# Performance work log

Measured on AMD Instinct MI355X. Metric: run time of the kernel, lower is better.

The kernel has to match this reference:

```python
import jax, jax.numpy as jnp
import numpy as np

N = 50000      # nodes
E = 800000     # edges
T = 3          # npass
ED = 64        # embedding_dim
NS = 23        # nshifts (arange(0.8, 3.0+1e-5, 0.1))
MD = NS + ED   # message_dim = 87
H = 200        # hidden width (hardcoded in module)
NMOL = 2048    # number of molecules (segments for final scatter)
RD = ED * (T + 1)  # readout input dim = 256
EPS = 1e-5

SHIFTS = jnp.asarray(np.arange(0.8, 3.0 + 1e-5, 0.1, dtype=np.float32))  # [23]


def setup_inputs() -> dict:
    key = jax.random.key(0)
    ks = jax.random.split(key, 32)
    inp = {
        'z_i': jax.random.randint(ks[0], (N,), 0, 10),
        'edge_index': jax.random.randint(ks[1], (2, E), 0, N),
        'dist_ij': jax.random.uniform(ks[2], (E, 1), dtype=jnp.float32) * 2.2 + 0.8,
        'mol_ind': jnp.sort(jax.random.randint(ks[3], (N,), 0, NMOL)),
        'emb': jax.random.normal(ks[4], (10, ED), dtype=jnp.float32),
        # per-pass update MLP params, stacked over T
        'up_bn_g': jnp.ones((T, MD), jnp.float32),
        'up_bn_b': jnp.zeros((T, MD), jnp.float32),
        'up_w1': jax.random.normal(ks[5], (T, MD, H), jnp.float32) * 0.05,
        'up_b1': jnp.zeros((T, H), jnp.float32),
        'up_w2': jax.random.normal(ks[6], (T, H, H), jnp.float32) * 0.05,
        'up_b2': jnp.zeros((T, H), jnp.float32),
        'up_w3': jax.random.normal(ks[7], (T, H, H), jnp.float32) * 0.05,
        'up_b3': jnp.zeros((T, H), jnp.float32),
        'up_w4': jax.random.normal(ks[8], (T, H, ED), jnp.float32) * 0.05,
        'up_b4': jnp.zeros((T, ED), jnp.float32),
        # readout MLP params
        'ro_bn_g': jnp.ones((RD,), jnp.float32),
        'ro_bn_b': jnp.zeros((RD,), jnp.float32),
        'ro_w1': jax.random.normal(ks[9], (RD, H), jnp.float32) * 0.05,
        'ro_b1': jnp.zeros((H,), jnp.float32),
        'ro_w2': jax.random.normal(ks[10], (H, H), jnp.float32) * 0.05,
        'ro_b2': jnp.zeros((H,), jnp.float32),
        'ro_w3': jax.random.normal(ks[11], (H, H), jnp.float32) * 0.05,
        'ro_b3': jnp.zeros((H,), jnp.float32),
        'ro_w4': jax.random.normal(ks[12], (H, 1), jnp.float32) * 0.05,
        'ro_b4': jnp.zeros((1,), jnp.float32),  # bias filled to 0 in __init__
    }
    return inp


def batchnorm(x, g, b):
    # BatchNorm1d in training mode: batch statistics, biased variance
    mu = jnp.mean(x, axis=0)
    var = jnp.mean(jnp.square(x - mu), axis=0)
    return (x - mu) * jax.lax.rsqrt(var + EPS) * g + b


def mlp(x, g, b, w1, b1, w2, b2, w3, b3, w4, b4):
    x = batchnorm(x, g, b)
    x = jax.nn.relu(x @ w1 + b1)
    x = jax.nn.relu(x @ w2 + b2)
    x = jax.nn.relu(x @ w3 + b3)
    return x @ w4 + b4


def reference(z_i, edge_index, dist_ij, mol_ind, emb,
              up_bn_g, up_bn_b, up_w1, up_b1, up_w2, up_b2, up_w3, up_b3, up_w4, up_b4,
              ro_bn_g, ro_bn_b, ro_w1, ro_b1, ro_w2, ro_b2, ro_w3, ro_b3, ro_w4, ro_b4):
    e_source, e_sink = edge_index[0], edge_index[1]
    rbf_ij = jnp.exp(-jnp.square(dist_ij - SHIFTS[None, :]))  # [E, NS]
    x_i = emb[z_i]                                            # [N, ED]
    x_list = [x_i]
    for t in range(T):
        m_ij = jnp.concatenate([rbf_ij, x_i[e_sink]], axis=1)  # [E, MD] gather
        m_i = jax.ops.segment_sum(m_ij, e_source, num_segments=N)  # scatter-sum
        x_i = x_i + 0.1 * mlp(m_i, up_bn_g[t], up_bn_b[t],
                              up_w1[t], up_b1[t], up_w2[t], up_b2[t],
                              up_w3[t], up_b3[t], up_w4[t], up_b4[t])
        x_list.append(x_i)
    x_all = jnp.concatenate(x_list, axis=1)  # [N, RD]
    y_i = mlp(x_all, ro_bn_g, ro_bn_b, ro_w1, ro_b1, ro_w2, ro_b2, ro_w3, ro_b3, ro_w4, ro_b4)
    y = jax.ops.segment_sum(y_i, mol_ind, num_segments=NMOL)  # [NMOL, 1]
    return y
```

## Files before the change

kernel.cpp:

```cpp
#include <hip/hip_runtime.h>
#include <hip/hip_bf16.h>
#include <type_traits>

#define NN 50000
#define NP 50048
#define EE 800000
#define TT 3
#define ED 64
#define NS 23
#define MD 87
#define HH 200
#define NMOL 2048
#define RD 256

#define SW 264
#define NPB2 512
#define SNB ((NN + 255) / 256)

typedef __attribute__((ext_vector_type(8))) short short8b;
typedef __attribute__((ext_vector_type(4))) float f32x4;

template <int V> using ic = std::integral_constant<int, V>;

__device__ __forceinline__ unsigned short f2bf(float f) {
  unsigned u = __float_as_uint(f);
  return (unsigned short)((u + 0x7fffu + ((u >> 16) & 1u)) >> 16);
}
__device__ __forceinline__ float ubf2f(unsigned short h) {
  return __uint_as_float(((unsigned)h) << 16);
}
__device__ __forceinline__ float bfp2f(unsigned p) {
  return __uint_as_float(p << 16) + __uint_as_float(p & 0xffff0000u);
}
__device__ __forceinline__ unsigned packsplit(float v) {
  unsigned short h = f2bf(v);
  unsigned short l = f2bf(v - ubf2f(h));
  return (unsigned)h | ((unsigned)l << 16);
}

__device__ __forceinline__ void gl2lds16(const short* g, short* l) {
  __builtin_amdgcn_global_load_lds(
      (const __attribute__((address_space(1))) unsigned int*)g,
      (__attribute__((address_space(3))) unsigned int*)l, 16, 0, 0);
}

__device__ __forceinline__ void vmwait(int n) {
  switch (n) {
    case 0: asm volatile("s_waitcnt vmcnt(0)" ::: "memory"); break;
    case 1: asm volatile("s_waitcnt vmcnt(1)" ::: "memory"); break;
    case 2: asm volatile("s_waitcnt vmcnt(2)" ::: "memory"); break;
    case 3: asm volatile("s_waitcnt vmcnt(3)" ::: "memory"); break;
    default: asm volatile("s_waitcnt vmcnt(4)" ::: "memory"); break;
  }
}

struct WD { const float* src; short* dst; int K, N, Kpad, Npad, T; };
struct WDs { WD d[5]; };

__global__ __launch_bounds__(256) void wprep_kernel(WDs W) {
  WD w = W.d[blockIdx.y];
  int KB = w.Kpad >> 5, NT = w.Npad >> 4;
  int per = w.Npad * w.Kpad;
  int total = w.T * per;
  for (int idx = blockIdx.x * 256 + threadIdx.x; idx < total; idx += gridDim.x * 256) {
    int t = idx / per;
    int r = idx - t * per;
    int e = r & 7, lane = (r >> 3) & 63;
    int blk = r >> 9;
    int kb = blk % KB, tile = blk / KB;
    int ln = lane & 15, quad = lane >> 4;
    int n = tile * 16 + ln, k = kb * 32 + quad * 8 + e;
    float v = 0.f;
    if (k < w.K && n < w.N) v = w.src[((size_t)t * w.K + k) * w.N + n];
    unsigned short h = f2bf(v);
    unsigned short l = f2bf(v - ubf2f(h));
    size_t base = ((size_t)(t * NT + tile) * KB + kb) * 1024;
    w.dst[base + lane * 8 + e] = (short)h;
    w.dst[base + 512 + lane * 8 + e] = (short)l;
  }
}

__global__ __launch_bounds__(256) void wscale_kernel(const float* __restrict__ wsrc,
                                                     const float* __restrict__ na,
                                                     const float* __restrict__ nb,
                                                     const float* __restrict__ bsrc,
                                                     int K, int Kpad,
                                                     short* __restrict__ wsp,
                                                     float* __restrict__ bc) {
  int n = blockIdx.x;
  int k = threadIdx.x;
  int KB = Kpad >> 5;
  int tile = n >> 4, ln = n & 15;
  float contrib = 0.f;
  if (k < Kpad) {
    float v = 0.f;
    if (n < HH && k < K) {
      float w = wsrc[(size_t)k * HH + n];
      v = na[k] * w;
      contrib = nb[k] * w;
    }
    unsigned short h = f2bf(v);
    unsigned short l = f2bf(v - ubf2f(h));
    int kb = k >> 5, quad = (k & 31) >> 3, e = k & 7;
    int lane = quad * 16 + ln;
    size_t base = ((size_t)tile * KB + kb) * 1024;
    wsp[base + lane * 8 + e] = (short)h;
    wsp[base + 512 + lane * 8 + e] = (short)l;
  }
  __shared__ float sh[256];
  sh[k] = contrib;
  __syncthreads();
  for (int off = 128; off > 0; off >>= 1) {
    if (k < off) sh[k] += sh[k + off];
    __syncthreads();
  }
  if (k == 0) bc[n] = (n < HH ? bsrc[n] : 0.f) + sh[0];
}

__global__ __launch_bounds__(256) void emb_kernel(const int* __restrict__ z,
                                                  const float* __restrict__ emb,
                                                  unsigned* __restrict__ xp,
                                                  short* __restrict__ xq,
                                                  short* __restrict__ xqs) {
  int idx = blockIdx.x * 256 + threadIdx.x;
  if (idx >= NN * ED) return;
  int i = idx >> 6, d = idx & 63;
  unsigned pk = packsplit(emb[z[i] * ED + d]);
  xp[(size_t)i * RD + d] = pk;
  short h = (short)(pk & 0xffffu);
  xq[(size_t)i * RD + d] = h;
  xqs[(size_t)i * ED + d] = h;
}

__global__ __launch_bounds__(256) void hist_kernel(const int* __restrict__ src,
                                                   int* __restrict__ deg) {
  int e = blockIdx.x * 256 + threadIdx.x;
  if (e < EE) atomicAdd(&deg[src[e]], 1);
}

__global__ __launch_bounds__(256) void scanA_kernel(const int* __restrict__ deg,
                                                    int* __restrict__ Psum) {
  int i = blockIdx.x * 256 + threadIdx.x;
  int v = (i < NN) ? deg[i] : 0;
#pragma unroll
  for (int off = 32; off > 0; off >>= 1) v += __shfl_down(v, off, 64);
  __shared__ int ws[4];
  if ((threadIdx.x & 63) == 0) ws[threadIdx.x >> 6] = v;
  __syncthreads();
  if (threadIdx.x == 0) Psum[blockIdx.x] = ws[0] + ws[1] + ws[2] + ws[3];
}

__global__ __launch_bounds__(256) void scanB_kernel(const int* __restrict__ Psum,
                                                    int* __restrict__ Poff) {
  __shared__ int sh[256];
  int t = threadIdx.x;
  int v = (t < SNB) ? Psum[t] : 0;
  sh[t] = v;
  __syncthreads();
  for (int off = 1; off < 256; off <<= 1) {
    int u = (t >= off) ? sh[t - off] : 0;
    __syncthreads();
    sh[t] += u;
    __syncthreads();
  }
  if (t < SNB) Poff[t] = sh[t] - v;
}

__global__ __launch_bounds__(256) void scanC_kernel(const int* __restrict__ deg,
                                                    const int* __restrict__ Poff,
                                                    int* __restrict__ offs,
                                                    int* __restrict__ cursor) {
  __shared__ int sh[256];
  int t = threadIdx.x;
  int i = blockIdx.x * 256 + t;
  int v = (i < NN) ? deg[i] : 0;
  sh[t] = v;
  __syncthreads();
  for (int off = 1; off < 256; off <<= 1) {
    int u = (t >= off) ? sh[t - off] : 0;
    __syncthreads();
    sh[t] += u;
    __syncthreads();
  }
  int excl = Poff[blockIdx.x] + sh[t] - v;
  if (i < NN) {
    offs[i] = excl;
    cursor[i] = excl;
    if (i == NN - 1) offs[NN] = excl + v;
  }
}

__global__ __launch_bounds__(256) void scatter_kernel(const int* __restrict__ src,
                                                      const int* __restrict__ snk,
                                                      const float* __restrict__ dist,
                                                      int* __restrict__ cursor,
                                                      int* __restrict__ ssink,
                                                      float* __restrict__ sdist) {
  int e = blockIdx.x * 256 + threadIdx.x;
  if (e >= EE) return;
  int p = atomicAdd(&cursor[src[e]], 1);
  ssink[p] = snk[e];
  sdist[p] = dist[e];
}

template <bool RBF>
__global__ __launch_bounds__(256) void gather_kernel(const int* __restrict__ offs,
                                                     const int* __restrict__ ssink,
                                                     const float* __restrict__ sdist,
                                                     const short* __restrict__ xqs,
                                                     short* __restrict__ mh) {
  int node = blockIdx.x * 4 + (threadIdx.x >> 6);
  int lane = threadIdx.x & 63;
  if (node >= NN) return;
  float shift = (float)(0.8 + 0.1 * (double)lane);
  int e0 = offs[node], e1 = offs[node + 1];
  float ax0 = 0.f, ax1 = 0.f, ar0 = 0.f, ar1 = 0.f;
  int j = e0;
  for (; j + 4 <= e1; j += 4) {
    int s0 = ssink[j], s1 = ssink[j + 1], s2 = ssink[j + 2], s3 = ssink[j + 3];
    float x0 = ubf2f((unsigned short)xqs[(size_t)s0 * ED + lane]);
    float x1 = ubf2f((unsigned short)xqs[(size_t)s1 * ED + lane]);
    float x2 = ubf2f((unsigned short)xqs[(size_t)s2 * ED + lane]);
    float x3 = ubf2f((unsigned short)xqs[(size_t)s3 * ED + lane]);
    ax0 += x0 + x2;
    ax1 += x1 + x3;
    if (RBF && lane < NS) {
      float d0 = sdist[j], d1 = sdist[j + 1], d2 = sdist[j + 2], d3 = sdist[j + 3];
      float u0 = d0 - shift, u1 = d1 - shift, u2 = d2 - shift, u3 = d3 - shift;
      ar0 += __expf(-u0 * u0) + __expf(-u2 * u2);
      ar1 += __expf(-u1 * u1) + __expf(-u3 * u3);
    }
  }
  for (; j < e1; j++) {
    int s = ssink[j];
    ax0 += ubf2f((unsigned short)xqs[(size_t)s * ED + lane]);
    if (RBF && lane < NS) {
      float u = sdist[j] - shift;
      ar0 += __expf(-u * u);
    }
  }
  float accx = ax0 + ax1;
  if (RBF && lane < NS) mh[(size_t)node * 96 + lane] = (short)f2bf(ar0 + ar1);
  if (RBF && lane >= NS && lane < 32) mh[(size_t)node * 96 + 64 + lane] = 0;
  mh[(size_t)node * 96 + NS + lane] = (short)f2bf(accx);
}

template <int LD>
__global__ __launch_bounds__(256) void colstats_s16_kernel(const short* __restrict__ X,
                                                           float* __restrict__ P) {
  constexpr int CG = LD / 8;
  constexpr int RPB = 256 / CG;
  const int t = threadIdx.x;
  const int cg = t % CG, rin = t / CG;
  float s[8] = {0, 0, 0, 0, 0, 0, 0, 0}, q[8] = {0, 0, 0, 0, 0, 0, 0, 0};
  if (rin < RPB) {
    for (int r = blockIdx.x * RPB + rin; r < NN; r += gridDim.x * RPB) {
      union { uint4 v; short e[8]; } u;
      u.v = *(const uint4*)(X + (size_t)r * LD + cg * 8);
#pragma unroll
      for (int e = 0; e < 8; e++) {
        float f = ubf2f((unsigned short)u.e[e]);
        s[e] += f;
        q[e] += f * f;
      }
    }
  }
  __shared__ float sh[256][16];
#pragma unroll
  for (int e = 0; e < 8; e++) { sh[t][e] = s[e]; sh[t][8 + e] = q[e]; }
  __syncthreads();
  if (rin == 0) {
    for (int rr = 1; rr < RPB; rr++) {
      const float* o = sh[rr * CG + cg];
#pragma unroll
      for (int e = 0; e < 8; e++) { s[e] += o[e]; q[e] += o[8 + e]; }
    }
    float* Pb = P + blockIdx.x * 512;
#pragma unroll
    for (int e = 0; e < 8; e++) {
      Pb[cg * 8 + e] = s[e];
      Pb[256 + cg * 8 + e] = q[e];
    }
  }
}

__global__ __launch_bounds__(256) void bnfinal2_kernel(const float* __restrict__ P, int nblk,
                                                       const float* __restrict__ g,
                                                       const float* __restrict__ b, int ncols,
                                                       float* __restrict__ na,
                                                       float* __restrict__ nb) {
  int c = blockIdx.x;
  int t = threadIdx.x;
  float s = 0.f, q = 0.f;
  for (int i = t; i < nblk; i += 256) {
    s += P[i * 512 + c];
    q += P[i * 512 + 256 + c];
  }
#pragma unroll
  for (int off = 32; off > 0; off >>= 1) {
    s += __shfl_down(s, off, 64);
    q += __shfl_down(q, off, 64);
  }
  __shared__ float ws[4], wq[4];
  if ((t & 63) == 0) { ws[t >> 6] = s; wq[t >> 6] = q; }
  __syncthreads();
  if (t == 0) {
    s = ws[0] + ws[1] + ws[2] + ws[3];
    q = wq[0] + wq[1] + wq[2] + wq[3];
    if (c < ncols) {
      float mean = s / (float)NN;
      float var = q / (float)NN - mean * mean;
      float a = g[c] * rsqrtf(var + 1e-5f);
      na[c] = a;
      nb[c] = b[c] - mean * a;
    } else {
      na[c] = 0.f;
      nb[c] = 0.f;
    }
  }
}

template <bool READOUT>
__global__ __launch_bounds__(256, 2) void fused_kernel(
    const short* __restrict__ Agh,
    const short* __restrict__ W1p, const short* __restrict__ W2p,
    const short* __restrict__ W3p, const short* __restrict__ W4p,
    const float* __restrict__ b1, const float* __restrict__ b2,
    const float* __restrict__ b3, const float* __restrict__ b4,
    unsigned* __restrict__ xp, short* __restrict__ xq, short* __restrict__ xqs,
    int t, const float* __restrict__ w4ro, const int* __restrict__ mol,
    float* __restrict__ out) {
  __shared__ short act[64 * SW];
  __shared__ short bufW[3][13 * 512];
  constexpr int GLDA = READOUT ? RD : 96;
  constexpr int KB1 = READOUT ? 8 : 3;
  const int tid = threadIdx.x;
  const int wave = tid >> 6, lane = tid & 63, ln = lane & 15, quad = lane >> 4;
  const int q8 = quad * 8;
  const int bm = blockIdx.x * 64;

  if constexpr (!READOUT) {
#pragma unroll
    for (int i = 0; i < 3; i++) {
      int idx = tid + 256 * i;
      int row = idx / 12, col = (idx - row * 12) * 8;
      *(uint4*)(act + row * SW + col) =
          *(const uint4*)(Agh + (size_t)(bm + row) * GLDA + col);
    }
    {
      int row = tid >> 2, c = 208 + (tid & 3) * 4;
      *(uint2*)(act + row * SW + c) = (uint2){0u, 0u};
    }
  } else {
#pragma unroll
    for (int i = 0; i < 8; i++) {
      int idx = tid + 256 * i;
      int row = idx >> 5, col = (idx & 31) * 8;
      *(uint4*)(act + row * SW + col) =
          *(const uint4*)(Agh + (size_t)(bm + row) * GLDA + col);
    }
  }
  __syncthreads();

  f32x4 acc[4][4];
  short8b a[4];

  auto stage = [&](const short* __restrict__ Wp, int NT, int KB, int TERMS,
                   int s, int bi) {
    int kb = (TERMS == 2) ? (s >> 1) : s;
    int pl = (TERMS == 2) ? ((s & 1) << 9) : 0;
    short* dst = &bufW[bi][0];
#pragma unroll
    for (int j = 0; j < 4; j++) {
      int tile = wave + 4 * j;
      if (tile < NT)
        gl2lds16(Wp + (size_t)(tile * KB + kb) * 1024 + pl + lane * 8,
                 dst + tile * 512);
    }
  };

  auto runloop = [&](auto ntt, auto kbt, auto tt, const short* __restrict__ Wp) {
    constexpr int NT = decltype(ntt)::value;
    constexpr int KB = decltype(kbt)::value;
    constexpr int TERMS = decltype(tt)::value;
    constexpr int NSL = KB * TERMS;
    constexpr int NJ = (NT + 3) >> 2;
    const int ntw = (NT - wave + 3) >> 2;
#pragma unroll
    for (int j = 0; j < NJ; j++)
#pragma unroll
      for (int i = 0; i < 4; i++) acc[j][i] = (f32x4){0.f, 0.f, 0.f, 0.f};
#pragma unroll
    for (int s = 0; s < NSL; s++) {
      vmwait((s < NSL - 1) ? ntw : 0);
      __builtin_amdgcn_s_barrier();
      __builtin_amdgcn_sched_barrier(0);
      if (s + 2 < NSL) stage(Wp, NT, KB, TERMS, s + 2, (s + 2) % 3);
      if (TERMS == 1 || (s & 1) == 0) {
        const int kb = (TERMS == 2) ? (s >> 1) : s;
#pragma unroll
        for (int i = 0; i < 4; i++)
          a[i] = *(const short8b*)(act + (i * 16 + ln) * SW + kb * 32 + q8);
      }
      const short* bw = &bufW[s % 3][0];
#pragma unroll
      for (int j = 0; j < NJ; j++) {
        int tile = wave + 4 * j;
        if (tile < NT) {
          short8b b = *(const short8b*)(bw + tile * 512 + lane * 8);
#pragma unroll
          for (int i = 0; i < 4; i++)
            acc[j][i] =
                __builtin_amdgcn_mfma_f32_16x16x32_bf16(a[i], b, acc[j][i], 0, 0, 0);
        }
      }
    }
  };

  auto epi = [&](auto ntt, const float* __restrict__ bias) {
    constexpr int NT = decltype(ntt)::value;
    constexpr int NJ = (NT + 3) >> 2;
#pragma unroll
    for (int j = 0; j < NJ; j++) {
      int tile = wave + 4 * j;
      if (tile < NT) {
        int colg = tile * 16 + ln;
        float bb = (colg < HH) ? bias[colg] : 0.f;
#pragma unroll
        for (int i = 0; i < 4; i++)
#pragma unroll
          for (int r = 0; r < 4; r++)
            act[(i * 16 + quad * 4 + r) * SW + colg] =
                (short)f2bf(fmaxf(acc[j][i][r] + bb, 0.f));
      }
    }
  };

  auto lgkmbar = [&]() {
    asm volatile("s_waitcnt lgkmcnt(0)" ::: "memory");
    __builtin_amdgcn_s_barrier();
    __builtin_amdgcn_sched_barrier(0);
  };

  stage(W1p, 13, KB1, 2, 0, 0);
  stage(W1p, 13, KB1, 2, 1, 1);
  runloop(ic<13>{}, ic<KB1>{}, ic<2>{}, W1p);
  __builtin_amdgcn_s_barrier();
  __builtin_amdgcn_sched_barrier(0);
  stage(W2p, 13, 7, 1, 0, 0);
  stage(W2p, 13, 7, 1, 1, 1);
  epi(ic<13>{}, b1);
  lgkmbar();

  runloop(ic<13>{}, ic<7>{}, ic<1>{}, W2p);
  __builtin_amdgcn_s_barrier();
  __builtin_amdgcn_sched_barrier(0);
  stage(W3p, 13, 7, 1, 0, 0);
  stage(W3p, 13, 7, 1, 1, 1);
  epi(ic<13>{}, b2);
  lgkmbar();

  runloop(ic<13>{}, ic<7>{}, ic<1>{}, W3p);
  __builtin_amdgcn_s_barrier();
  __builtin_amdgcn_sched_barrier(0);

  if constexpr (!READOUT) {
    stage(W4p, 4, 7, 2, 0, 0);
    stage(W4p, 4, 7, 2, 1, 1);
    epi(ic<13>{}, b3);
    lgkmbar();
    runloop(ic<4>{}, ic<7>{}, ic<2>{}, W4p);
    int colg = wave * 16 + ln;
    float bb = b4[colg];
#pragma unroll
    for (int i = 0; i < 4; i++)
#pragma unroll
      for (int r = 0; r < 4; r++) {
        int grow = bm + i * 16 + quad * 4 + r;
        if (grow < NN) {
          size_t base = (size_t)grow * RD;
          float oldv = bfp2f(xp[base + (size_t)t * ED + colg]);
          unsigned pk = packsplit(oldv + 0.1f * (acc[0][i][r] + bb));
          xp[base + (size_t)(t + 1) * ED + colg] = pk;
          short h = (short)(pk & 0xffffu);
          xq[base + (size_t)(t + 1) * ED + colg] = h;
          xqs[(size_t)(t + 1) * NN * ED + (size_t)grow * ED + colg] = h;
        }
      }
  } else {
    epi(ic<13>{}, b3);
    lgkmbar();
    int row = tid >> 2;
    float s = 0.f;
    for (int c = (tid & 3); c < HH; c += 4)
      s += ubf2f((unsigned short)act[row * SW + c]) * w4ro[c];
    s += __shfl_xor(s, 1, 64);
    s += __shfl_xor(s, 2, 64);
    int grow = bm + row;
    if ((tid & 3) == 0 && grow < NN) atomicAdd(&out[mol[grow]], s + b4[0]);
  }
}

extern "C" void kernel_launch(void* const* d_in, const int* in_sizes, int n_in,
                              void* d_out, int out_size, void* d_ws, size_t ws_size,
                              hipStream_t stream) {
  const int* z_i = (const int*)d_in[0];
  const int* e_src = (const int*)d_in[1];
  const int* e_snk = ((const int*)d_in[1]) + EE;
  const float* dist = (const float*)d_in[2];
  const int* mol = (const int*)d_in[3];
  const float* emb = (const float*)d_in[4];
  const float* up_bn_g = (const float*)d_in[5];
  const float* up_bn_b = (const float*)d_in[6];
  const float* up_w1 = (const float*)d_in[7];
  const float* up_b1 = (const float*)d_in[8];
  const float* up_w2 = (const float*)d_in[9];
  const float* up_b2 = (const float*)d_in[10];
  const float* up_w3 = (const float*)d_in[11];
  const float* up_b3 = (const float*)d_in[12];
  const float* up_w4 = (const float*)d_in[13];
  const float* up_b4 = (const float*)d_in[14];
  const float* ro_bn_g = (const float*)d_in[15];
  const float* ro_bn_b = (const float*)d_in[16];
  const float* ro_w1 = (const float*)d_in[17];
  const float* ro_b1 = (const float*)d_in[18];
  const float* ro_w2 = (const float*)d_in[19];
  const float* ro_b2 = (const float*)d_in[20];
  const float* ro_w3 = (const float*)d_in[21];
  const float* ro_b3 = (const float*)d_in[22];
  const float* ro_w4 = (const float*)d_in[23];
  const float* ro_b4 = (const float*)d_in[24];
  float* out = (float*)d_out;

  char* p = (char*)d_ws;
  auto alloc = [&](size_t bytes) {
    void* r = (void*)p;
    p += (bytes + 255) & ~(size_t)255;
    return r;
  };
  unsigned* x_p = (unsigned*)alloc((size_t)NN * RD * 4);
  short* x_q = (short*)alloc((size_t)NP * RD * 2);
  short* x_qs = (short*)alloc((size_t)(TT + 1) * NN * ED * 2);
  short* mh = (short*)alloc((size_t)NP * 96 * 2);
  int* ssink = (int*)alloc((size_t)EE * 4);
  float* sdist = (float*)alloc((size_t)EE * 4);
  int* offs = (int*)alloc((size_t)(NN + 1) * 4);
  int* deg = (int*)alloc((size_t)NN * 4);
  int* cursor = (int*)alloc((size_t)NN * 4);
  int* Psum = (int*)alloc((size_t)SNB * 4);
  int* Poff = (int*)alloc((size_t)SNB * 4);
  float* P = (float*)alloc((size_t)NPB2 * 512 * 4);
  float* na = (float*)alloc(256 * 4);
  float* nb = (float*)alloc(256 * 4);
  float* b1c = (float*)alloc(208 * 4);
  short* w1sp = (short*)alloc((size_t)13 * 3 * 1024 * 2);
  short* r1sp = (short*)alloc((size_t)13 * 8 * 1024 * 2);
  short* w2p = (short*)alloc((size_t)TT * 13 * 7 * 1024 * 2);
  short* w3p = (short*)alloc((size_t)TT * 13 * 7 * 1024 * 2);
  short* w4p = (short*)alloc((size_t)TT * 4 * 7 * 1024 * 2);
  short* r2p = (short*)alloc((size_t)13 * 7 * 1024 * 2);
  short* r3p = (short*)alloc((size_t)13 * 7 * 1024 * 2);

  hipMemsetAsync(deg, 0, (size_t)NN * 4, stream);
  hipMemsetAsync(out, 0, (size_t)NMOL * 4, stream);

  WDs descs;
  descs.d[0] = {up_w2, w2p, HH, HH, 224, 208, TT};
  descs.d[1] = {up_w3, w3p, HH, HH, 224, 208, TT};
  descs.d[2] = {up_w4, w4p, HH, ED, 224, 64, TT};
  descs.d[3] = {ro_w2, r2p, HH, HH, 224, 208, 1};
  descs.d[4] = {ro_w3, r3p, HH, HH, 224, 208, 1};
  wprep_kernel<<<dim3(546, 5), 256, 0, stream>>>(descs);

  emb_kernel<<<(NN * ED + 255) / 256, 256, 0, stream>>>(z_i, emb, x_p, x_q, x_qs);
  hist_kernel<<<(EE + 255) / 256, 256, 0, stream>>>(e_src, deg);
  scanA_kernel<<<SNB, 256, 0, stream>>>(deg, Psum);
  scanB_kernel<<<1, 256, 0, stream>>>(Psum, Poff);
  scanC_kernel<<<SNB, 256, 0, stream>>>(deg, Poff, offs, cursor);
  scatter_kernel<<<(EE + 255) / 256, 256, 0, stream>>>(e_src, e_snk, dist, cursor, ssink, sdist);

  const int gM = NP / 64;

  for (int t = 0; t < TT; t++) {
    if (t == 0)
      gather_kernel<true><<<(NN + 3) / 4, 256, 0, stream>>>(
          offs, ssink, sdist, x_qs, mh);
    else
      gather_kernel<false><<<(NN + 3) / 4, 256, 0, stream>>>(
          offs, ssink, sdist, x_qs + (size_t)t * NN * ED, mh);
    colstats_s16_kernel<96><<<NPB2, 256, 0, stream>>>(mh, P);
    bnfinal2_kernel<<<256, 256, 0, stream>>>(P, NPB2, up_bn_g + t * MD, up_bn_b + t * MD, MD,
                                             na, nb);
    wscale_kernel<<<208, 256, 0, stream>>>(up_w1 + (size_t)t * MD * HH, na, nb,
                                           up_b1 + t * HH, MD, 96, w1sp, b1c);
    fused_kernel<false><<<gM, 256, 0, stream>>>(
        mh, w1sp,
        w2p + (size_t)t * 13 * 7 * 1024, w3p + (size_t)t * 13 * 7 * 1024,
        w4p + (size_t)t * 4 * 7 * 1024,
        b1c, up_b2 + t * HH, up_b3 + t * HH, up_b4 + t * ED,
        x_p, x_q, x_qs, t, nullptr, nullptr, nullptr);
  }

  colstats_s16_kernel<256><<<NPB2, 256, 0, stream>>>(x_q, P);
  bnfinal2_kernel<<<256, 256, 0, stream>>>(P, NPB2, ro_bn_g, ro_bn_b, RD, na, nb);
  wscale_kernel<<<208, 256, 0, stream>>>(ro_w1, na, nb, ro_b1, RD, 256, r1sp, b1c);
  fused_kernel<true><<<gM, 256, 0, stream>>>(
      x_q, r1sp, r2p, r3p, nullptr,
      b1c, ro_b2, ro_b3, ro_b4,
      nullptr, nullptr, nullptr, 0, ro_w4, mol, out);

  (void)in_sizes; (void)n_in; (void)out_size; (void)ws_size;
}
```

Measured before the change: 612.7 us.

## Simplify fused MLP pipeline to double buffering with higher occupancy

Replaces the triple-buffered, template-specialized weight pipeline with a runtime-parameterized double-buffered loop synchronized by __syncthreads each step. It shrinks the activation stride and weight buffers to cut LDS usage and raises the occupancy hint to three blocks per CU. The first layer now reads A fragments directly from global memory instead of staging them in LDS. It trades explicit vmcnt-based overlap and compile-time unrolling for lower LDS footprint, risking less latency hiding and possible async-load ordering issues.

```diff
diff --git a/kernel.cpp b/kernel.cpp
--- a/kernel.cpp
+++ b/kernel.cpp
@@ -13,14 +13,12 @@
 #define NMOL 2048
 #define RD 256
 
-#define SW 264
+#define SW 216
 #define NPB2 512
 #define SNB ((NN + 255) / 256)
 
 typedef __attribute__((ext_vector_type(8))) short short8b;
 typedef __attribute__((ext_vector_type(4))) float f32x4;
-
-template <int V> using ic = std::integral_constant<int, V>;
 
 __device__ __forceinline__ unsigned short f2bf(float f) {
   unsigned u = __float_as_uint(f);
@@ -42,16 +40,6 @@
   __builtin_amdgcn_global_load_lds(
       (const __attribute__((address_space(1))) unsigned int*)g,
       (__attribute__((address_space(3))) unsigned int*)l, 16, 0, 0);
-}
-
-__device__ __forceinline__ void vmwait(int n) {
-  switch (n) {
-    case 0: asm volatile("s_waitcnt vmcnt(0)" ::: "memory"); break;
-    case 1: asm volatile("s_waitcnt vmcnt(1)" ::: "memory"); break;
-    case 2: asm volatile("s_waitcnt vmcnt(2)" ::: "memory"); break;
-    case 3: asm volatile("s_waitcnt vmcnt(3)" ::: "memory"); break;
-    default: asm volatile("s_waitcnt vmcnt(4)" ::: "memory"); break;
-  }
 }
 
 struct WD { const float* src; short* dst; int K, N, Kpad, Npad, T; };
@@ -321,7 +309,7 @@
 }
 
 template <bool READOUT>
-__global__ __launch_bounds__(256, 2) void fused_kernel(
+__global__ __launch_bounds__(256, 3) void fused_kernel(
     const short* __restrict__ Agh,
     const short* __restrict__ W1p, const short* __restrict__ W2p,
     const short* __restrict__ W3p, const short* __restrict__ W4p,
@@ -331,7 +319,7 @@
     int t, const float* __restrict__ w4ro, const int* __restrict__ mol,
     float* __restrict__ out) {
   __shared__ short act[64 * SW];
-  __shared__ short bufW[3][13 * 512];
+  __shared__ short bufW[2][13 * 512];
   constexpr int GLDA = READOUT ? RD : 96;
   constexpr int KB1 = READOUT ? 8 : 3;
   const int tid = threadIdx.x;
@@ -339,72 +327,48 @@
   const int q8 = quad * 8;
   const int bm = blockIdx.x * 64;
 
-  if constexpr (!READOUT) {
-#pragma unroll
-    for (int i = 0; i < 3; i++) {
-      int idx = tid + 256 * i;
-      int row = idx / 12, col = (idx - row * 12) * 8;
-      *(uint4*)(act + row * SW + col) =
-          *(const uint4*)(Agh + (size_t)(bm + row) * GLDA + col);
-    }
-    {
-      int row = tid >> 2, c = 208 + (tid & 3) * 4;
-      *(uint2*)(act + row * SW + c) = (uint2){0u, 0u};
-    }
-  } else {
-#pragma unroll
-    for (int i = 0; i < 8; i++) {
-      int idx = tid + 256 * i;
-      int row = idx >> 5, col = (idx & 31) * 8;
-      *(uint4*)(act + row * SW + col) =
-          *(const uint4*)(Agh + (size_t)(bm + row) * GLDA + col);
-    }
-  }
-  __syncthreads();
-
   f32x4 acc[4][4];
-  short8b a[4];
+  const short8b zfrag = {0, 0, 0, 0, 0, 0, 0, 0};
 
   auto stage = [&](const short* __restrict__ Wp, int NT, int KB, int TERMS,
-                   int s, int bi) {
+                   int s, int b) {
     int kb = (TERMS == 2) ? (s >> 1) : s;
     int pl = (TERMS == 2) ? ((s & 1) << 9) : 0;
-    short* dst = &bufW[bi][0];
 #pragma unroll
     for (int j = 0; j < 4; j++) {
       int tile = wave + 4 * j;
       if (tile < NT)
         gl2lds16(Wp + (size_t)(tile * KB + kb) * 1024 + pl + lane * 8,
-                 dst + tile * 512);
+                 &bufW[b][tile * 512]);
     }
   };
 
-  auto runloop = [&](auto ntt, auto kbt, auto tt, const short* __restrict__ Wp) {
-    constexpr int NT = decltype(ntt)::value;
-    constexpr int KB = decltype(kbt)::value;
-    constexpr int TERMS = decltype(tt)::value;
-    constexpr int NSL = KB * TERMS;
-    constexpr int NJ = (NT + 3) >> 2;
-    const int ntw = (NT - wave + 3) >> 2;
-#pragma unroll
-    for (int j = 0; j < NJ; j++)
+  auto runloop = [&](const short* __restrict__ AG, const short* __restrict__ Wp,
+                     int NT, int KB, int TERMS) {
+    const int NSL = KB * TERMS;
+#pragma unroll
+    for (int j = 0; j < 4; j++)
 #pragma unroll
       for (int i = 0; i < 4; i++) acc[j][i] = (f32x4){0.f, 0.f, 0.f, 0.f};
-#pragma unroll
-    for (int s = 0; s < NSL; s++) {
-      vmwait((s < NSL - 1) ? ntw : 0);
-      __builtin_amdgcn_s_barrier();
-      __builtin_amdgcn_sched_barrier(0);
-      if (s + 2 < NSL) stage(Wp, NT, KB, TERMS, s + 2, (s + 2) % 3);
-      if (TERMS == 1 || (s & 1) == 0) {
-        const int kb = (TERMS == 2) ? (s >> 1) : s;
+    for (int s = 0; s < NSL; ++s) {
+      if (s + 1 < NSL) stage(Wp, NT, KB, TERMS, s + 1, (s + 1) & 1);
+      int kb = (TERMS == 2) ? (s >> 1) : s;
+      short8b a[4];
+      if (AG) {
 #pragma unroll
         for (int i = 0; i < 4; i++)
-          a[i] = *(const short8b*)(act + (i * 16 + ln) * SW + kb * 32 + q8);
+          a[i] = *(const short8b*)(AG + (size_t)(bm + i * 16 + ln) * GLDA +
+                                   kb * 32 + q8);
+      } else {
+        int col = kb * 32 + q8;
+#pragma unroll
+        for (int i = 0; i < 4; i++)
+          a[i] = (col < 208) ? *(const short8b*)(act + (i * 16 + ln) * SW + col)
+                             : zfrag;
       }
-      const short* bw = &bufW[s % 3][0];
-#pragma unroll
-      for (int j = 0; j < NJ; j++) {
+      const short* bw = &bufW[s & 1][0];
+#pragma unroll
+      for (int j = 0; j < 4; j++) {
         int tile = wave + 4 * j;
         if (tile < NT) {
           short8b b = *(const short8b*)(bw + tile * 512 + lane * 8);
@@ -414,16 +378,15 @@
                 __builtin_amdgcn_mfma_f32_16x16x32_bf16(a[i], b, acc[j][i], 0, 0, 0);
         }
       }
+      __syncthreads();
     }
   };
 
-  auto epi = [&](auto ntt, const float* __restrict__ bias) {
-    constexpr int NT = decltype(ntt)::value;
-    constexpr int NJ = (NT + 3) >> 2;
-#pragma unroll
-    for (int j = 0; j < NJ; j++) {
+  auto epi = [&](const float* __restrict__ bias) {
+#pragma unroll
+    for (int j = 0; j < 4; j++) {
       int tile = wave + 4 * j;
-      if (tile < NT) {
+      if (tile < 13) {
         int colg = tile * 16 + ln;
         float bb = (colg < HH) ? bias[colg] : 0.f;
 #pragma unroll
@@ -436,40 +399,25 @@
     }
   };
 
-  auto lgkmbar = [&]() {
-    asm volatile("s_waitcnt lgkmcnt(0)" ::: "memory");
-    __builtin_amdgcn_s_barrier();
-    __builtin_amdgcn_sched_barrier(0);
-  };
-
   stage(W1p, 13, KB1, 2, 0, 0);
-  stage(W1p, 13, KB1, 2, 1, 1);
-  runloop(ic<13>{}, ic<KB1>{}, ic<2>{}, W1p);
-  __builtin_amdgcn_s_barrier();
-  __builtin_amdgcn_sched_barrier(0);
+  __syncthreads();
+  runloop(Agh, W1p, 13, KB1, 2);
   stage(W2p, 13, 7, 1, 0, 0);
-  stage(W2p, 13, 7, 1, 1, 1);
-  epi(ic<13>{}, b1);
-  lgkmbar();
-
-  runloop(ic<13>{}, ic<7>{}, ic<1>{}, W2p);
-  __builtin_amdgcn_s_barrier();
-  __builtin_amdgcn_sched_barrier(0);
+  epi(b1);
+  __syncthreads();
+
+  runloop(nullptr, W2p, 13, 7, 1);
   stage(W3p, 13, 7, 1, 0, 0);
-  stage(W3p, 13, 7, 1, 1, 1);
-  epi(ic<13>{}, b2);
-  lgkmbar();
-
-  runloop(ic<13>{}, ic<7>{}, ic<1>{}, W3p);
-  __builtin_amdgcn_s_barrier();
-  __builtin_amdgcn_sched_barrier(0);
+  epi(b2);
+  __syncthreads();
+
+  runloop(nullptr, W3p, 13, 7, 1);
 
   if constexpr (!READOUT) {
     stage(W4p, 4, 7, 2, 0, 0);
-    stage(W4p, 4, 7, 2, 1, 1);
-    epi(ic<13>{}, b3);
-    lgkmbar();
-    runloop(ic<4>{}, ic<7>{}, ic<2>{}, W4p);
+    epi(b3);
+    __syncthreads();
+    runloop(nullptr, W4p, 4, 7, 2);
     int colg = wave * 16 + ln;
     float bb = b4[colg];
 #pragma unroll
@@ -488,8 +436,8 @@
         }
       }
   } else {
-    epi(ic<13>{}, b3);
-    lgkmbar();
+    epi(b3);
+    __syncthreads();
     int row = tid >> 2;
     float s = 0.f;
     for (int c = (tid & 3); c < HH; c += 4)
```

Result: slower. 632.2 us (+3.2%).
